# Kernel optimization log

Measured on AMD Instinct MI355X. Metric: run time of the kernel, lower is better.

The kernel has to match this reference:

```python
import jax, jax.numpy as jnp
import numpy as np

N_NODES = 100000
N_EDGES = 3200000


def gcn_conv(x, W, b, src, dst, n_nodes):
    """PyG GCNConv: self-loops, symmetric D^-1/2 A D^-1/2 norm, linear, bias."""
    loop = jnp.arange(n_nodes, dtype=src.dtype)
    s = jnp.concatenate([src, loop])  # [E+N]
    d = jnp.concatenate([dst, loop])  # [E+N]
    # degree computed at destination (col), edge_weight = 1
    deg = jax.ops.segment_sum(jnp.ones_like(d, dtype=x.dtype), d,
                              num_segments=n_nodes)
    dinv = jnp.where(deg > 0, jax.lax.rsqrt(deg), 0.0)
    norm = dinv[s] * dinv[d]  # [E+N]
    h = x @ W.T  # [N, out]
    msg = h[s] * norm[:, None]  # gather + scale, [E+N, out]
    out = jax.ops.segment_sum(msg, d, num_segments=n_nodes)  # scatter-add
    return out + b


def setup_inputs() -> dict:
    key = jax.random.key(0)
    k1, k2, k3, k4 = jax.random.split(key, 4)
    x = jax.random.normal(k1, (N_NODES, 2), dtype=jnp.float32)
    edge_index = jax.random.randint(k2, (2, N_EDGES), 0, N_NODES,
                                    dtype=jnp.int64)
    # Glorot-ish init for linear weights
    W1 = jax.random.normal(k3, (64, 2), dtype=jnp.float32) * 0.5
    b1 = jnp.zeros((64,), dtype=jnp.float32)
    W2 = jax.random.normal(k4, (2, 64), dtype=jnp.float32) * 0.125
    b2 = jnp.zeros((2,), dtype=jnp.float32)
    return {"x": x, "edge_index": edge_index, "W1": W1, "b1": b1,
            "W2": W2, "b2": b2}


def reference(x, edge_index, W1, b1, W2, b2):
    src, dst = edge_index[0], edge_index[1]
    h = gcn_conv(x, W1, b1, src, dst, N_NODES)
    h = jax.nn.relu(h)
    out = gcn_conv(h, W2, b2, src, dst, N_NODES)
    return out
```

## Files before the change

### kernel.cpp

```cpp
#include <hip/hip_runtime.h>

#define N_NODES 100000
#define SHIFT 9
#define BNODES 512
#define NB 196
#define CAP 18432
#define TILE 4096
#define SB 256


__global__ __launch_bounds__(SB) void k_sort(const int* __restrict__ src,
                                             const int* __restrict__ dst,
                                             int* claim, int* sg, int e) {
    __shared__ int hist[NB];
    __shared__ int cnt[SB];
    __shared__ int start[NB];
    __shared__ int runbase[NB];
    __shared__ int stage[TILE];
    __shared__ unsigned char binmap[TILE];

    const int t = threadIdx.x;
    const int base = blockIdx.x * TILE;
    const int n = min(TILE, e - base);

    for (int i = t; i < NB; i += SB) hist[i] = 0;
    __syncthreads();

    int recs[16];
    int bins[16];
#pragma unroll
    for (int k = 0; k < 4; ++k) {
        int idx = base + (k * SB + t) * 4;
        if (idx + 3 < e) {
            int4 s4 = *(const int4*)(src + idx);
            int4 d4 = *(const int4*)(dst + idx);
            int ss[4] = {s4.x, s4.y, s4.z, s4.w};
            int dd[4] = {d4.x, d4.y, d4.z, d4.w};
#pragma unroll
            for (int j = 0; j < 4; ++j) {
                int b = dd[j] >> SHIFT;
                bins[4 * k + j] = b;
                recs[4 * k + j] = ss[j] | ((dd[j] & (BNODES - 1)) << 17);
                atomicAdd(&hist[b], 1);
            }
        } else {
#pragma unroll
            for (int j = 0; j < 4; ++j) {
                int i2 = idx + j;
                if (i2 < e) {
                    int d = dst[i2];
                    int b = d >> SHIFT;
                    bins[4 * k + j] = b;
                    recs[4 * k + j] = src[i2] | ((d & (BNODES - 1)) << 17);
                    atomicAdd(&hist[b], 1);
                } else {
                    bins[4 * k + j] = -1;
                }
            }
        }
    }
    __syncthreads();

    cnt[t] = (t < NB) ? hist[t] : 0;
    __syncthreads();
    for (int off = 1; off < SB; off <<= 1) {
        int w = (t >= off) ? cnt[t - off] : 0;
        __syncthreads();
        cnt[t] += w;
        __syncthreads();
    }
    if (t < NB) {
        int excl = cnt[t] - hist[t];
        start[t] = excl;
        cnt[t] = excl;
        int c = hist[t];
        runbase[t] = c ? atomicAdd(&claim[t], c) : 0;
    }
    __syncthreads();

#pragma unroll
    for (int m = 0; m < 16; ++m) {
        int b = bins[m];
        if (b >= 0) {
            int pos = atomicAdd(&cnt[b], 1);
            stage[pos] = recs[m];
            binmap[pos] = (unsigned char)b;
        }
    }
    __syncthreads();

    for (int i = t; i < n; i += SB) {
        int b = binmap[i];
        sg[b * CAP + runbase[b] + (i - start[b])] = stage[i];
    }
}

__global__ __launch_bounds__(1024) void k_refine(const int* __restrict__ claim,
                                                 const int* __restrict__ sg,
                                                 const float* __restrict__ x,
                                                 int* sg2, int* beg, int* endv,
                                                 float2* u) {
    __shared__ int hist[BNODES];
    __shared__ int excl[BNODES];
    const int t = threadIdx.x;
    const int b = blockIdx.x;
    if (t < BNODES) hist[t] = 0;
    __syncthreads();

    const int* p = sg + b * CAP;
    const int len = claim[b];
    const int tb = len & ~3;
    for (int i = 4 * t; i < tb; i += 4096) {
        int4 r = *(const int4*)(p + i);
        atomicAdd(&hist[((unsigned)r.x) >> 17], 1);
        atomicAdd(&hist[((unsigned)r.y) >> 17], 1);
        atomicAdd(&hist[((unsigned)r.z) >> 17], 1);
        atomicAdd(&hist[((unsigned)r.w) >> 17], 1);
    }
    if (t < len - tb) atomicAdd(&hist[((unsigned)p[tb + t]) >> 17], 1);
    __syncthreads();

    if (t < BNODES) excl[t] = hist[t];
    __syncthreads();
    for (int off = 1; off < BNODES; off <<= 1) {
        int w = (t >= off && t < BNODES) ? excl[t - off] : 0;
        __syncthreads();
        if (t < BNODES) excl[t] += w;
        __syncthreads();
    }

    int myexcl = 0;
    if (t < BNODES) {
        int mycnt = hist[t];
        myexcl = excl[t] - mycnt;
        int node = b * BNODES + t;
        if (node < N_NODES) {
            beg[node]  = b * CAP + myexcl;
            endv[node] = b * CAP + myexcl + mycnt;
            float dv = rsqrtf((float)(mycnt + 1));
            float2 xv = ((const float2*)x)[node];
            u[node] = make_float2(dv * xv.x, dv * xv.y);
        }
    }
    __syncthreads();
    if (t < BNODES) hist[t] = myexcl;
    __syncthreads();

    int* q = sg2 + b * CAP;
    for (int i = 4 * t; i < tb; i += 4096) {
        int4 r = *(const int4*)(p + i);
        q[atomicAdd(&hist[((unsigned)r.x) >> 17], 1)] = r.x & 0x1FFFF;
        q[atomicAdd(&hist[((unsigned)r.y) >> 17], 1)] = r.y & 0x1FFFF;
        q[atomicAdd(&hist[((unsigned)r.z) >> 17], 1)] = r.z & 0x1FFFF;
        q[atomicAdd(&hist[((unsigned)r.w) >> 17], 1)] = r.w & 0x1FFFF;
    }
    if (t < len - tb) {
        int r = p[tb + t];
        q[atomicAdd(&hist[((unsigned)r) >> 17], 1)] = r & 0x1FFFF;
    }
}

__global__ __launch_bounds__(256) void k_agg1(const int* __restrict__ sg2,
                                              const int* __restrict__ beg,
                                              const int* __restrict__ endv,
                                              const float2* __restrict__ u,
                                              const float* __restrict__ W1,
                                              const float* __restrict__ b1,
                                              const float* __restrict__ W2,
                                              float2* v) {
    __shared__ float sW1[128], sb1[64], sW2[128];
    int t = threadIdx.x;
    if (t < 128) { sW1[t] = W1[t]; sW2[t] = W2[t]; }
    else if (t < 192) sb1[t - 128] = b1[t - 128];
    __syncthreads();
    int n = blockIdx.x * 256 + t;
    if (n >= N_NODES) return;
    int s = beg[n], e2 = endv[n];
    float sx = 0.f, sy = 0.f;
    int i = s;
    for (; i + 4 <= e2; i += 4) {
        int r0 = sg2[i], r1 = sg2[i + 1], r2 = sg2[i + 2], r3 = sg2[i + 3];
        float2 g0 = u[r0], g1 = u[r1], g2 = u[r2], g3 = u[r3];
        sx += (g0.x + g1.x) + (g2.x + g3.x);
        sy += (g0.y + g1.y) + (g2.y + g3.y);
    }
    for (; i < e2; ++i) { float2 g = u[sg2[i]]; sx += g.x; sy += g.y; }
    float dv = rsqrtf((float)(e2 - s + 1));
    float2 un = u[n];
    float a0 = dv * (sx + un.x), a1 = dv * (sy + un.y);
    float y0 = 0.f, y1 = 0.f;
#pragma unroll
    for (int j = 0; j < 64; ++j) {
        float h = fmaxf(fmaf(sW1[2 * j], a0,
                        fmaf(sW1[2 * j + 1], a1, sb1[j])), 0.f);
        y0 = fmaf(sW2[j], h, y0);
        y1 = fmaf(sW2[64 + j], h, y1);
    }
    v[n] = make_float2(dv * y0, dv * y1);
}

__global__ __launch_bounds__(256) void k_agg2(const int* __restrict__ sg2,
                                              const int* __restrict__ beg,
                                              const int* __restrict__ endv,
                                              const float2* __restrict__ v,
                                              const float* __restrict__ b2,
                                              float2* out) {
    int n = blockIdx.x * 256 + threadIdx.x;
    if (n >= N_NODES) return;
    int s = beg[n], e2 = endv[n];
    float sx = 0.f, sy = 0.f;
    int i = s;
    for (; i + 4 <= e2; i += 4) {
        int r0 = sg2[i], r1 = sg2[i + 1], r2 = sg2[i + 2], r3 = sg2[i + 3];
        float2 g0 = v[r0], g1 = v[r1], g2 = v[r2], g3 = v[r3];
        sx += (g0.x + g1.x) + (g2.x + g3.x);
        sy += (g0.y + g1.y) + (g2.y + g3.y);
    }
    for (; i < e2; ++i) { float2 g = v[sg2[i]]; sx += g.x; sy += g.y; }
    float dv = rsqrtf((float)(e2 - s + 1));
    float2 vn = v[n];
    out[n] = make_float2(fmaf(dv, sx + vn.x, b2[0]),
                         fmaf(dv, sy + vn.y, b2[1]));
}

extern "C" void kernel_launch(void* const* d_in, const int* in_sizes, int n_in,
                              void* d_out, int out_size, void* d_ws, size_t ws_size,
                              hipStream_t stream) {
    const float* x  = (const float*)d_in[0];
    const int* ei   = (const int*)d_in[1];
    const float* W1 = (const float*)d_in[2];
    const float* b1 = (const float*)d_in[3];
    const float* W2 = (const float*)d_in[4];
    const float* b2 = (const float*)d_in[5];

    int e = in_sizes[1] / 2;
    const int* src = ei;
    const int* dst = ei + e;

    int* ws      = (int*)d_ws;
    int* claim   = ws;
    int* sg      = ws + NB;
    int* sg2     = sg + NB * CAP;
    int* beg     = sg2 + NB * CAP;
    int* endv    = beg + N_NODES;
    float2* u    = (float2*)(endv + N_NODES);
    float2* v    = u + N_NODES;
    float2* outp = (float2*)d_out;

    hipMemsetAsync(claim, 0, NB * sizeof(int), stream);

    const int gN = (N_NODES + 255) / 256;
    k_sort  <<<(e + TILE - 1) / TILE, SB, 0, stream>>>(src, dst, claim, sg, e);
    k_refine<<<NB, 1024, 0, stream>>>(claim, sg, x, sg2, beg, endv, u);
    k_agg1  <<<gN, 256, 0, stream>>>(sg2, beg, endv, u, W1, b1, W2, v);
    k_agg2  <<<gN, 256, 0, stream>>>(sg2, beg, endv, v, b2, outp);
}
```

Baseline: 166.0 us.

## Enlarge sort tiles, register-cache refine records, pack node ranges, unroll gathers by eight

```diff
diff --git a/kernel.cpp b/kernel.cpp
--- a/kernel.cpp
+++ b/kernel.cpp
@@ -5,15 +5,15 @@
 #define BNODES 512
 #define NB 196
 #define CAP 18432
-#define TILE 4096
-#define SB 256
+#define TILE 8192
+#define SB 512
 
 
 __global__ __launch_bounds__(SB) void k_sort(const int* __restrict__ src,
                                              const int* __restrict__ dst,
                                              int* claim, int* sg, int e) {
     __shared__ int hist[NB];
-    __shared__ int cnt[SB];
+    __shared__ int scanb[256];
     __shared__ int start[NB];
     __shared__ int runbase[NB];
     __shared__ int stage[TILE];
@@ -61,19 +61,19 @@
     }
     __syncthreads();
 
-    cnt[t] = (t < NB) ? hist[t] : 0;
-    __syncthreads();
-    for (int off = 1; off < SB; off <<= 1) {
-        int w = (t >= off) ? cnt[t - off] : 0;
-        __syncthreads();
-        cnt[t] += w;
+    if (t < 256) scanb[t] = (t < NB) ? hist[t] : 0;
+    __syncthreads();
+    for (int off = 1; off < 256; off <<= 1) {
+        int w = (t < 256 && t >= off) ? scanb[t - off] : 0;
+        __syncthreads();
+        if (t < 256) scanb[t] += w;
         __syncthreads();
     }
     if (t < NB) {
-        int excl = cnt[t] - hist[t];
+        int c = hist[t];
+        int excl = scanb[t] - c;
         start[t] = excl;
-        cnt[t] = excl;
-        int c = hist[t];
+        scanb[t] = excl;
         runbase[t] = c ? atomicAdd(&claim[t], c) : 0;
     }
     __syncthreads();
@@ -82,7 +82,7 @@
     for (int m = 0; m < 16; ++m) {
         int b = bins[m];
         if (b >= 0) {
-            int pos = atomicAdd(&cnt[b], 1);
+            int pos = atomicAdd(&scanb[b], 1);
             stage[pos] = recs[m];
             binmap[pos] = (unsigned char)b;
         }
@@ -98,71 +98,73 @@
 __global__ __launch_bounds__(1024) void k_refine(const int* __restrict__ claim,
                                                  const int* __restrict__ sg,
                                                  const float* __restrict__ x,
-                                                 int* sg2, int* beg, int* endv,
+                                                 int* sg2, int* packed,
                                                  float2* u) {
     __shared__ int hist[BNODES];
-    __shared__ int excl[BNODES];
+    __shared__ int scanb[BNODES];
     const int t = threadIdx.x;
     const int b = blockIdx.x;
-    if (t < BNODES) hist[t] = 0;
-    __syncthreads();
-
     const int* p = sg + b * CAP;
     const int len = claim[b];
-    const int tb = len & ~3;
-    for (int i = 4 * t; i < tb; i += 4096) {
-        int4 r = *(const int4*)(p + i);
-        atomicAdd(&hist[((unsigned)r.x) >> 17], 1);
-        atomicAdd(&hist[((unsigned)r.y) >> 17], 1);
-        atomicAdd(&hist[((unsigned)r.z) >> 17], 1);
-        atomicAdd(&hist[((unsigned)r.w) >> 17], 1);
-    }
-    if (t < len - tb) atomicAdd(&hist[((unsigned)p[tb + t]) >> 17], 1);
-    __syncthreads();
-
-    if (t < BNODES) excl[t] = hist[t];
+
+    int4 r[5];
+#pragma unroll
+    for (int k = 0; k < 5; ++k) {
+        int idx = 4 * t + 4096 * k;
+        int4 v = make_int4(-1, -1, -1, -1);
+        if (idx + 3 < len) v = *(const int4*)(p + idx);
+        else if (idx < len) {
+            v.x = p[idx];
+            if (idx + 1 < len) v.y = p[idx + 1];
+            if (idx + 2 < len) v.z = p[idx + 2];
+        }
+        r[k] = v;
+    }
+    if (t < BNODES) hist[t] = 0;
+    __syncthreads();
+#pragma unroll
+    for (int k = 0; k < 5; ++k) {
+        if (r[k].x != -1) atomicAdd(&hist[((unsigned)r[k].x) >> 17], 1);
+        if (r[k].y != -1) atomicAdd(&hist[((unsigned)r[k].y) >> 17], 1);
+        if (r[k].z != -1) atomicAdd(&hist[((unsigned)r[k].z) >> 17], 1);
+        if (r[k].w != -1) atomicAdd(&hist[((unsigned)r[k].w) >> 17], 1);
+    }
+    __syncthreads();
+
+    if (t < BNODES) scanb[t] = hist[t];
     __syncthreads();
     for (int off = 1; off < BNODES; off <<= 1) {
-        int w = (t >= off && t < BNODES) ? excl[t - off] : 0;
-        __syncthreads();
-        if (t < BNODES) excl[t] += w;
-        __syncthreads();
-    }
-
-    int myexcl = 0;
+        int w = (t >= off && t < BNODES) ? scanb[t - off] : 0;
+        __syncthreads();
+        if (t < BNODES) scanb[t] += w;
+        __syncthreads();
+    }
     if (t < BNODES) {
         int mycnt = hist[t];
-        myexcl = excl[t] - mycnt;
+        int myexcl = scanb[t] - mycnt;
         int node = b * BNODES + t;
         if (node < N_NODES) {
-            beg[node]  = b * CAP + myexcl;
-            endv[node] = b * CAP + myexcl + mycnt;
+            packed[node] = (b * CAP + myexcl) | (mycnt << 22);
             float dv = rsqrtf((float)(mycnt + 1));
             float2 xv = ((const float2*)x)[node];
             u[node] = make_float2(dv * xv.x, dv * xv.y);
         }
-    }
-    __syncthreads();
-    if (t < BNODES) hist[t] = myexcl;
+        hist[t] = myexcl;
+    }
     __syncthreads();
 
     int* q = sg2 + b * CAP;
-    for (int i = 4 * t; i < tb; i += 4096) {
-        int4 r = *(const int4*)(p + i);
-        q[atomicAdd(&hist[((unsigned)r.x) >> 17], 1)] = r.x & 0x1FFFF;
-        q[atomicAdd(&hist[((unsigned)r.y) >> 17], 1)] = r.y & 0x1FFFF;
-        q[atomicAdd(&hist[((unsigned)r.z) >> 17], 1)] = r.z & 0x1FFFF;
-        q[atomicAdd(&hist[((unsigned)r.w) >> 17], 1)] = r.w & 0x1FFFF;
-    }
-    if (t < len - tb) {
-        int r = p[tb + t];
-        q[atomicAdd(&hist[((unsigned)r) >> 17], 1)] = r & 0x1FFFF;
+#pragma unroll
+    for (int k = 0; k < 5; ++k) {
+        if (r[k].x != -1) q[atomicAdd(&hist[((unsigned)r[k].x) >> 17], 1)] = r[k].x & 0x1FFFF;
+        if (r[k].y != -1) q[atomicAdd(&hist[((unsigned)r[k].y) >> 17], 1)] = r[k].y & 0x1FFFF;
+        if (r[k].z != -1) q[atomicAdd(&hist[((unsigned)r[k].z) >> 17], 1)] = r[k].z & 0x1FFFF;
+        if (r[k].w != -1) q[atomicAdd(&hist[((unsigned)r[k].w) >> 17], 1)] = r[k].w & 0x1FFFF;
     }
 }
 
 __global__ __launch_bounds__(256) void k_agg1(const int* __restrict__ sg2,
-                                              const int* __restrict__ beg,
-                                              const int* __restrict__ endv,
+                                              const int* __restrict__ packed,
                                               const float2* __restrict__ u,
                                               const float* __restrict__ W1,
                                               const float* __restrict__ b1,
@@ -175,17 +177,22 @@
     __syncthreads();
     int n = blockIdx.x * 256 + t;
     if (n >= N_NODES) return;
-    int s = beg[n], e2 = endv[n];
+    int pk = packed[n];
+    int s = pk & 0x3FFFFF;
+    int cnt = ((unsigned)pk) >> 22;
+    int e2 = s + cnt;
     float sx = 0.f, sy = 0.f;
     int i = s;
-    for (; i + 4 <= e2; i += 4) {
-        int r0 = sg2[i], r1 = sg2[i + 1], r2 = sg2[i + 2], r3 = sg2[i + 3];
-        float2 g0 = u[r0], g1 = u[r1], g2 = u[r2], g3 = u[r3];
-        sx += (g0.x + g1.x) + (g2.x + g3.x);
-        sy += (g0.y + g1.y) + (g2.y + g3.y);
+    for (; i + 8 <= e2; i += 8) {
+        float2 g0 = u[sg2[i]],     g1 = u[sg2[i + 1]];
+        float2 g2 = u[sg2[i + 2]], g3 = u[sg2[i + 3]];
+        float2 g4 = u[sg2[i + 4]], g5 = u[sg2[i + 5]];
+        float2 g6 = u[sg2[i + 6]], g7 = u[sg2[i + 7]];
+        sx += ((g0.x + g1.x) + (g2.x + g3.x)) + ((g4.x + g5.x) + (g6.x + g7.x));
+        sy += ((g0.y + g1.y) + (g2.y + g3.y)) + ((g4.y + g5.y) + (g6.y + g7.y));
     }
     for (; i < e2; ++i) { float2 g = u[sg2[i]]; sx += g.x; sy += g.y; }
-    float dv = rsqrtf((float)(e2 - s + 1));
+    float dv = rsqrtf((float)(cnt + 1));
     float2 un = u[n];
     float a0 = dv * (sx + un.x), a1 = dv * (sy + un.y);
     float y0 = 0.f, y1 = 0.f;
@@ -200,24 +207,28 @@
 }
 
 __global__ __launch_bounds__(256) void k_agg2(const int* __restrict__ sg2,
-                                              const int* __restrict__ beg,
-                                              const int* __restrict__ endv,
+                                              const int* __restrict__ packed,
                                               const float2* __restrict__ v,
                                               const float* __restrict__ b2,
                                               float2* out) {
     int n = blockIdx.x * 256 + threadIdx.x;
     if (n >= N_NODES) return;
-    int s = beg[n], e2 = endv[n];
+    int pk = packed[n];
+    int s = pk & 0x3FFFFF;
+    int cnt = ((unsigned)pk) >> 22;
+    int e2 = s + cnt;
     float sx = 0.f, sy = 0.f;
     int i = s;
-    for (; i + 4 <= e2; i += 4) {
-        int r0 = sg2[i], r1 = sg2[i + 1], r2 = sg2[i + 2], r3 = sg2[i + 3];
-        float2 g0 = v[r0], g1 = v[r1], g2 = v[r2], g3 = v[r3];
-        sx += (g0.x + g1.x) + (g2.x + g3.x);
-        sy += (g0.y + g1.y) + (g2.y + g3.y);
+    for (; i + 8 <= e2; i += 8) {
+        float2 g0 = v[sg2[i]],     g1 = v[sg2[i + 1]];
+        float2 g2 = v[sg2[i + 2]], g3 = v[sg2[i + 3]];
+        float2 g4 = v[sg2[i + 4]], g5 = v[sg2[i + 5]];
+        float2 g6 = v[sg2[i + 6]], g7 = v[sg2[i + 7]];
+        sx += ((g0.x + g1.x) + (g2.x + g3.x)) + ((g4.x + g5.x) + (g6.x + g7.x));
+        sy += ((g0.y + g1.y) + (g2.y + g3.y)) + ((g4.y + g5.y) + (g6.y + g7.y));
     }
     for (; i < e2; ++i) { float2 g = v[sg2[i]]; sx += g.x; sy += g.y; }
-    float dv = rsqrtf((float)(e2 - s + 1));
+    float dv = rsqrtf((float)(cnt + 1));
     float2 vn = v[n];
     out[n] = make_float2(fmaf(dv, sx + vn.x, b2[0]),
                          fmaf(dv, sy + vn.y, b2[1]));
@@ -241,9 +252,8 @@
     int* claim   = ws;
     int* sg      = ws + NB;
     int* sg2     = sg + NB * CAP;
-    int* beg     = sg2 + NB * CAP;
-    int* endv    = beg + N_NODES;
-    float2* u    = (float2*)(endv + N_NODES);
+    int* packed  = sg2 + NB * CAP;
+    float2* u    = (float2*)(packed + N_NODES);
     float2* v    = u + N_NODES;
     float2* outp = (float2*)d_out;
 
@@ -251,7 +261,7 @@
 
     const int gN = (N_NODES + 255) / 256;
     k_sort  <<<(e + TILE - 1) / TILE, SB, 0, stream>>>(src, dst, claim, sg, e);
-    k_refine<<<NB, 1024, 0, stream>>>(claim, sg, x, sg2, beg, endv, u);
-    k_agg1  <<<gN, 256, 0, stream>>>(sg2, beg, endv, u, W1, b1, W2, v);
-    k_agg2  <<<gN, 256, 0, stream>>>(sg2, beg, endv, v, b2, outp);
-}
+    k_refine<<<NB, 1024, 0, stream>>>(claim, sg, x, sg2, packed, u);
+    k_agg1  <<<gN, 256, 0, stream>>>(sg2, packed, u, W1, b1, W2, v);
+    k_agg2  <<<gN, 256, 0, stream>>>(sg2, packed, v, b2, outp);
+}
```

After: 159.3 us. 1.04x faster.
